# Kernel tuning notes

Measured on AMD Instinct MI355X. Metric: run time of the kernel, lower is better.

Reference implementation:

```python
import jax, jax.numpy as jnp
import numpy as np
import math

D = 768      # n_embd
NH = 12      # n_head
L = 4        # n_layer
E = 8        # num_experts
K = 2        # top_k
V = 50257    # vocab
H = 4 * D    # ffn hidden
MOE_LAYERS = (1, 3)


def _ln(x, g, b):
    m = x.mean(-1, keepdims=True)
    v = ((x - m) ** 2).mean(-1, keepdims=True)
    return (x - m) * jax.lax.rsqrt(v + 1e-5) * g + b


def setup_inputs() -> dict:
    key = jax.random.key(0)
    ks = iter(jax.random.split(key, 32))
    s = 0.02

    def rnd(shape):
        return jax.random.normal(next(ks), shape, dtype=jnp.float32) * s

    inp = {
        "x": jax.random.randint(next(ks), (2, 512), 0, V),
        "emb": rnd((V, D)),                       # tied embedding / output projection
        "wqkv": rnd((L, 3 * D, D)), "bqkv": jnp.zeros((L, 3 * D)),
        "wo": rnd((L, D, D)), "bo": jnp.zeros((L, D)),
        "ln1g": jnp.ones((L, D)), "ln1b": jnp.zeros((L, D)),
        "ln2g": jnp.ones((L, D)), "ln2b": jnp.zeros((L, D)),
        "sw1": rnd((2, H, D)), "sb1": jnp.zeros((2, H)),   # dense FFN layers (0, 2)
        "sw2": rnd((2, D, H)), "sb2": jnp.zeros((2, D)),
        "gw": rnd((2, E, D)),                              # router weights (layers 1, 3)
        "mw1": rnd((2, E, H, D)), "mb1": jnp.zeros((2, E, H)),
        "mw2": rnd((2, E, D, H)), "mb2": jnp.zeros((2, E, D)),
        "lnfg": jnp.ones((D,)), "lnfb": jnp.zeros((D,)),
    }
    return inp


def reference(x, emb, wqkv, bqkv, wo, bo, ln1g, ln1b, ln2g, ln2b,
              sw1, sb1, sw2, sb2, gw, mw1, mb1, mw2, mb2, lnfg, lnfb):
    b, t = x.shape
    dh = D // NH

    h = emb[x]  # [b,t,d]
    # sinusoidal positional encoding
    pos = jnp.arange(t, dtype=jnp.float32)[:, None]
    div = jnp.exp(jnp.arange(0, D, 2, dtype=jnp.float32) * (-math.log(10000.0) / D))
    pe = jnp.stack([jnp.sin(pos * div), jnp.cos(pos * div)], axis=-1).reshape(t, D)
    h = h + pe[None]

    # causal mask: query i cannot attend to key j > i
    neg = jnp.asarray(-jnp.inf, dtype=h.dtype)
    mask = jnp.where(jnp.arange(t)[None, :] > jnp.arange(t)[:, None], neg, 0.0)

    std_i = 0
    moe_i = 0
    for i in range(L):
        # pre-norm self-attention
        xn = _ln(h, ln1g[i], ln1b[i])
        qkv = xn @ wqkv[i].T + bqkv[i]          # [b,t,3d]
        q, k, v = jnp.split(qkv, 3, axis=-1)

        def heads(z):
            return z.reshape(b, t, NH, dh).transpose(0, 2, 1, 3)  # [b,nh,t,dh]

        q, k, v = heads(q), heads(k), heads(v)
        sc = jnp.einsum('bhqd,bhkd->bhqk', q, k) / math.sqrt(dh) + mask
        a = jax.nn.softmax(sc, axis=-1)
        o = jnp.einsum('bhqk,bhkd->bhqd', a, v).transpose(0, 2, 1, 3).reshape(b, t, D)
        h = h + o @ wo[i].T + bo[i]

        # pre-norm FFN (dense or MoE)
        xn = _ln(h, ln2g[i], ln2b[i])
        if i in MOE_LAYERS:
            T = b * t
            xf = xn.reshape(T, D)
            gl = xf @ gw[moe_i].T                      # router logits [T,E]
            probs = jax.nn.softmax(gl, axis=-1)
            topv, topi = jax.lax.top_k(probs, K)       # [T,K]
            w = topv / topv.sum(-1, keepdims=True)     # renormalized top-k gates
            cw = jnp.zeros_like(probs).at[jnp.arange(T)[:, None], topi].set(w)  # [T,E]
            he = jax.nn.gelu(jnp.einsum('td,ehd->teh', xf, mw1[moe_i]) + mb1[moe_i],
                             approximate=False)        # [T,E,H]
            ye = jnp.einsum('teh,edh->ted', he, mw2[moe_i]) + mb2[moe_i]        # [T,E,D]
            ff = jnp.einsum('ted,te->td', ye, cw).reshape(b, t, D)
            moe_i += 1
        else:
            ff = jax.nn.gelu(xn @ sw1[std_i].T + sb1[std_i], approximate=False) @ sw2[std_i].T + sb2[std_i]
            std_i += 1
        h = h + ff

    h = _ln(h, lnfg, lnfb)
    logits = h @ emb.T  # tied output projection, [b,t,V]
    return logits
```

## Files before the change

### kernel.cpp

```cpp
#include <hip/hip_runtime.h>
#include <hip/hip_bf16.h>
#include <cstdint>
#include <cstddef>

#define Dm   768
#define NHm  12
#define Lm   4
#define Em   8
#define Vm   50257
#define Hm   3072
#define Tm   512
#define Bm   2
#define NT   (Bm*Tm)
#define NAS  (NT*2)

typedef float f32x4 __attribute__((ext_vector_type(4)));
typedef short bf16x8 __attribute__((ext_vector_type(8)));

__device__ __forceinline__ float gelu_exact(float x) {
    return 0.5f * x * (1.0f + erff(x * 0.70710678118654752440f));
}

__device__ __forceinline__ unsigned short f2bf(float f) {
    __hip_bfloat16 h = __float2bfloat16(f);
    union { __hip_bfloat16 h; unsigned short s; } c; c.h = h; return c.s;
}
__device__ __forceinline__ float bf2f_bits(unsigned short b) {
    union { unsigned u; float f; } c; c.u = ((unsigned)b) << 16; return c.f;
}

__global__ __launch_bounds__(256) void cvt_bf16_kernel(const float* __restrict__ in,
                                                       unsigned short* __restrict__ out,
                                                       long n) {
    long i = ((long)blockIdx.x * 256 + threadIdx.x) * 8;
    if (i + 8 <= n) {
        const float4* s4 = reinterpret_cast<const float4*>(in + i);
        float4 f0 = s4[0], f1 = s4[1];
        union { unsigned short s[8]; uint4 v; } p;
        p.s[0] = f2bf(f0.x); p.s[1] = f2bf(f0.y); p.s[2] = f2bf(f0.z); p.s[3] = f2bf(f0.w);
        p.s[4] = f2bf(f1.x); p.s[5] = f2bf(f1.y); p.s[6] = f2bf(f1.z); p.s[7] = f2bf(f1.w);
        *reinterpret_cast<uint4*>(out + i) = p.v;
    } else {
        for (long j = i; j < n; ++j) out[j] = f2bf(in[j]);
    }
}

__global__ __launch_bounds__(256) void embed_kernel(const int* __restrict__ x,
                                                    const float* __restrict__ emb,
                                                    float* __restrict__ h) {
    int g = blockIdx.x;
    int tid = threadIdx.x;
    int tok = x[g];
    int pos = g % Tm;
    const float* erow = emb + (size_t)tok * Dm;
    for (int d = tid; d < Dm; d += 256) {
        int i2 = (d >> 1) * 2;
        float div = expf(-logf(10000.0f) * (float)i2 / (float)Dm);
        float a = (float)pos * div;
        float pe = (d & 1) ? cosf(a) : sinf(a);
        h[(size_t)g * Dm + d] = erow[d] + pe;
    }
}

__global__ __launch_bounds__(256) void ln_kernel(const float* __restrict__ in,
                                                 const float* __restrict__ g,
                                                 const float* __restrict__ b,
                                                 float* __restrict__ out) {
    int t = blockIdx.x, tid = threadIdx.x;
    const float* x = in + (size_t)t * Dm;
    float v0 = x[tid], v1 = x[tid + 256], v2 = x[tid + 512];
    __shared__ float red[256];
    red[tid] = v0 + v1 + v2;
    __syncthreads();
    for (int off = 128; off > 0; off >>= 1) {
        if (tid < off) red[tid] += red[tid + off];
        __syncthreads();
    }
    float mean = red[0] * (1.0f / Dm);
    __syncthreads();
    float d0 = v0 - mean, d1 = v1 - mean, d2 = v2 - mean;
    red[tid] = d0 * d0 + d1 * d1 + d2 * d2;
    __syncthreads();
    for (int off = 128; off > 0; off >>= 1) {
        if (tid < off) red[tid] += red[tid + off];
        __syncthreads();
    }
    float inv = rsqrtf(red[0] * (1.0f / Dm) + 1e-5f);
    float* o = out + (size_t)t * Dm;
    o[tid]       = d0 * inv * g[tid]       + b[tid];
    o[tid + 256] = d1 * inv * g[tid + 256] + b[tid + 256];
    o[tid + 512] = d2 * inv * g[tid + 512] + b[tid + 512];
}

#define MB 128
#define NB 128
#define KB 32
#define LDT 40

__device__ __forceinline__ void stage_tile(unsigned short* lds, const float* src,
                                           bool valid, int srow, int shalf) {
    union { unsigned short s[8]; uint4 v; } p0, p1;
    if (valid) {
        const float4* s4 = reinterpret_cast<const float4*>(src);
        #pragma unroll
        for (int q = 0; q < 4; ++q) {
            float4 f = s4[q];
            float vv[4] = {f.x, f.y, f.z, f.w};
            #pragma unroll
            for (int j = 0; j < 4; ++j) {
                int idx = q * 4 + j;
                unsigned short hb = f2bf(vv[j]);
                if (idx < 8) p0.s[idx] = hb; else p1.s[idx - 8] = hb;
            }
        }
    } else {
        p0.v = make_uint4(0, 0, 0, 0);
        p1.v = make_uint4(0, 0, 0, 0);
    }
    uint4* dst = reinterpret_cast<uint4*>(&lds[srow * LDT + shalf * 16]);
    dst[0] = p0.v; dst[1] = p1.v;
}

__device__ __forceinline__ void stage_tile_split(unsigned short* lds_hi,
                                                 unsigned short* lds_lo,
                                                 const float* src,
                                                 bool valid, int srow, int shalf) {
    union { unsigned short s[8]; uint4 v; } h0, h1, l0, l1;
    if (valid) {
        const float4* s4 = reinterpret_cast<const float4*>(src);
        #pragma unroll
        for (int q = 0; q < 4; ++q) {
            float4 f = s4[q];
            float vv[4] = {f.x, f.y, f.z, f.w};
            #pragma unroll
            for (int j = 0; j < 4; ++j) {
                int idx = q * 4 + j;
                unsigned short hb = f2bf(vv[j]);
                unsigned short lb = f2bf(vv[j] - bf2f_bits(hb));
                if (idx < 8) { h0.s[idx] = hb; l0.s[idx] = lb; }
                else         { h1.s[idx - 8] = hb; l1.s[idx - 8] = lb; }
            }
        }
    } else {
        h0.v = make_uint4(0,0,0,0); h1.v = make_uint4(0,0,0,0);
        l0.v = make_uint4(0,0,0,0); l1.v = make_uint4(0,0,0,0);
    }
    uint4* dh = reinterpret_cast<uint4*>(&lds_hi[srow * LDT + shalf * 16]);
    dh[0] = h0.v; dh[1] = h1.v;
    uint4* dl = reinterpret_cast<uint4*>(&lds_lo[srow * LDT + shalf * 16]);
    dl[0] = l0.v; dl[1] = l1.v;
}

__global__ __launch_bounds__(256) void mfma_gemm_bf(const unsigned short* __restrict__ A,
                                                    const unsigned short* __restrict__ B,
                                                    const float* __restrict__ bias,
                                                    float* __restrict__ C,
                                                    int M, int N, int K) {
    __shared__ __align__(16) unsigned short As[MB * LDT];
    __shared__ __align__(16) unsigned short Bs[NB * LDT];
    int tid = threadIdx.x;
    int nt_m = M / MB;
    int total = gridDim.x;
    int bid = blockIdx.x;
    int swz = bid;
    if ((total & 7) == 0) {
        int chunk = total >> 3;
        swz = (bid & 7) * chunk + (bid >> 3);
    }
    int bm = (swz % nt_m) * MB;
    int bn = (swz / nt_m) * NB;
    int srow = tid >> 1, shalf = tid & 1;
    int lane = tid & 63, w = tid >> 6;
    int wr = w >> 1, wc = w & 1;
    int r0 = (lane >> 4) * 4, c0 = lane & 15;
    int kb = (lane >> 4) * 8;

    bool bval = (bn + srow) < N;
    const unsigned short* Ap = A + (size_t)(bm + srow) * K + shalf * 16;
    const unsigned short* Bp = B + (size_t)(bn + srow) * K + shalf * 16;

    uint4 ra0, ra1, rb0, rb1;
    ra0 = reinterpret_cast<const uint4*>(Ap)[0];
    ra1 = reinterpret_cast<const uint4*>(Ap)[1];
    rb0 = make_uint4(0,0,0,0); rb1 = make_uint4(0,0,0,0);
    if (bval) {
        rb0 = reinterpret_cast<const uint4*>(Bp)[0];
        rb1 = reinterpret_cast<const uint4*>(Bp)[1];
    }

    f32x4 acc[4][4] = {};

    for (int kk = 0; kk < K; kk += KB) {
        uint4* da = reinterpret_cast<uint4*>(&As[srow * LDT + shalf * 16]);
        da[0] = ra0; da[1] = ra1;
        uint4* db = reinterpret_cast<uint4*>(&Bs[srow * LDT + shalf * 16]);
        db[0] = rb0; db[1] = rb1;
        __syncthreads();
        if (kk + KB < K) {
            const uint4* na = reinterpret_cast<const uint4*>(Ap + kk + KB);
            ra0 = na[0]; ra1 = na[1];
            if (bval) {
                const uint4* nb = reinterpret_cast<const uint4*>(Bp + kk + KB);
                rb0 = nb[0]; rb1 = nb[1];
            }
        }
        bf16x8 af[4], bf[4];
        #pragma unroll
        for (int m = 0; m < 4; ++m)
            af[m] = *reinterpret_cast<const bf16x8*>(&As[(wr * 64 + m * 16 + c0) * LDT + kb]);
        #pragma unroll
        for (int n = 0; n < 4; ++n)
            bf[n] = *reinterpret_cast<const bf16x8*>(&Bs[(wc * 64 + n * 16 + c0) * LDT + kb]);
        #pragma unroll
        for (int m = 0; m < 4; ++m)
            #pragma unroll
            for (int n = 0; n < 4; ++n)
                acc[m][n] = __builtin_amdgcn_mfma_f32_16x16x32_bf16(af[m], bf[n], acc[m][n], 0, 0, 0);
        __syncthreads();
    }

    #pragma unroll
    for (int n = 0; n < 4; ++n) {
        int col = bn + wc * 64 + n * 16 + c0;
        if (col < N) {
            float bv = bias ? bias[col] : 0.f;
            #pragma unroll
            for (int m = 0; m < 4; ++m)
                #pragma unroll
                for (int r = 0; r < 4; ++r) {
                    int row = bm + wr * 64 + m * 16 + r0 + r;
                    C[(size_t)row * N + col] = acc[m][n][r] + bv;
                }
        }
    }
}

template<int ACT, int RES>
__global__ __launch_bounds__(256) void mfma_gemm(const float* __restrict__ A,
                                                 const float* __restrict__ B,
                                                 const float* __restrict__ bias,
                                                 const float* __restrict__ res,
                                                 float* __restrict__ C,
                                                 int M, int N, int K) {
    __shared__ __align__(16) unsigned short As[MB * LDT];
    __shared__ __align__(16) unsigned short Bs[NB * LDT];
    int tid = threadIdx.x;
    int bm = blockIdx.y * MB, bn = blockIdx.x * NB;
    int srow = tid >> 1, shalf = tid & 1;
    int lane = tid & 63, w = tid >> 6;
    int wr = w >> 1, wc = w & 1;
    int r0 = (lane >> 4) * 4, c0 = lane & 15;
    int kb = (lane >> 4) * 8;

    f32x4 acc[4][4] = {};

    for (int kk = 0; kk < K; kk += KB) {
        stage_tile(As, A + (size_t)(bm + srow) * K + kk + shalf * 16, true, srow, shalf);
        bool bval = (bn + srow) < N;
        stage_tile(Bs, B + (size_t)(bn + srow) * K + kk + shalf * 16, bval, srow, shalf);
        __syncthreads();
        bf16x8 af[4], bf[4];
        #pragma unroll
        for (int m = 0; m < 4; ++m)
            af[m] = *reinterpret_cast<const bf16x8*>(&As[(wr * 64 + m * 16 + c0) * LDT + kb]);
        #pragma unroll
        for (int n = 0; n < 4; ++n)
            bf[n] = *reinterpret_cast<const bf16x8*>(&Bs[(wc * 64 + n * 16 + c0) * LDT + kb]);
        #pragma unroll
        for (int m = 0; m < 4; ++m)
            #pragma unroll
            for (int n = 0; n < 4; ++n)
                acc[m][n] = __builtin_amdgcn_mfma_f32_16x16x32_bf16(af[m], bf[n], acc[m][n], 0, 0, 0);
        __syncthreads();
    }

    #pragma unroll
    for (int n = 0; n < 4; ++n) {
        int col = bn + wc * 64 + n * 16 + c0;
        if (col < N) {
            float bv = bias ? bias[col] : 0.f;
            #pragma unroll
            for (int m = 0; m < 4; ++m) {
                #pragma unroll
                for (int r = 0; r < 4; ++r) {
                    int row = bm + wr * 64 + m * 16 + r0 + r;
                    float v = acc[m][n][r] + bv;
                    if (RES) v += res[(size_t)row * N + col];
                    if (ACT == 1) v = gelu_exact(v);
                    C[(size_t)row * N + col] = v;
                }
            }
        }
    }
}

__global__ __launch_bounds__(256) void mfma_gemm_sp_part(const float* __restrict__ A,
                                                         const float* __restrict__ B,
                                                         float* __restrict__ part,
                                                         int M, int N, int K, int KSPLIT) {
    __shared__ __align__(16) unsigned short Ah[MB * LDT];
    __shared__ __align__(16) unsigned short Al[MB * LDT];
    __shared__ __align__(16) unsigned short Bh[NB * LDT];
    __shared__ __align__(16) unsigned short Bl[NB * LDT];
    int tid = threadIdx.x;
    int bm = blockIdx.y * MB, bn = blockIdx.x * NB;
    int kc = blockIdx.z;
    int chunk = K / KSPLIT;
    int kbeg = kc * chunk;
    int srow = tid >> 1, shalf = tid & 1;
    int lane = tid & 63, w = tid >> 6;
    int wr = w >> 1, wc = w & 1;
    int r0 = (lane >> 4) * 4, c0 = lane & 15;
    int kb = (lane >> 4) * 8;

    f32x4 acc[4][4] = {};

    for (int kk = kbeg; kk < kbeg + chunk; kk += KB) {
        stage_tile_split(Ah, Al, A + (size_t)(bm + srow) * K + kk + shalf * 16, true, srow, shalf);
        stage_tile_split(Bh, Bl, B + (size_t)(bn + srow) * K + kk + shalf * 16, true, srow, shalf);
        __syncthreads();
        bf16x8 ah[4], al[4], bh[4], bl[4];
        #pragma unroll
        for (int m = 0; m < 4; ++m) {
            int o = (wr * 64 + m * 16 + c0) * LDT + kb;
            ah[m] = *reinterpret_cast<const bf16x8*>(&Ah[o]);
            al[m] = *reinterpret_cast<const bf16x8*>(&Al[o]);
        }
        #pragma unroll
        for (int n = 0; n < 4; ++n) {
            int o = (wc * 64 + n * 16 + c0) * LDT + kb;
            bh[n] = *reinterpret_cast<const bf16x8*>(&Bh[o]);
            bl[n] = *reinterpret_cast<const bf16x8*>(&Bl[o]);
        }
        #pragma unroll
        for (int m = 0; m < 4; ++m)
            #pragma unroll
            for (int n = 0; n < 4; ++n) {
                acc[m][n] = __builtin_amdgcn_mfma_f32_16x16x32_bf16(al[m], bh[n], acc[m][n], 0, 0, 0);
                acc[m][n] = __builtin_amdgcn_mfma_f32_16x16x32_bf16(ah[m], bl[n], acc[m][n], 0, 0, 0);
                acc[m][n] = __builtin_amdgcn_mfma_f32_16x16x32_bf16(ah[m], bh[n], acc[m][n], 0, 0, 0);
            }
        __syncthreads();
    }

    float* P = part + (size_t)kc * M * N;
    #pragma unroll
    for (int n = 0; n < 4; ++n) {
        int col = bn + wc * 64 + n * 16 + c0;
        #pragma unroll
        for (int m = 0; m < 4; ++m)
            #pragma unroll
            for (int r = 0; r < 4; ++r) {
                int row = bm + wr * 64 + m * 16 + r0 + r;
                P[(size_t)row * N + col] = acc[m][n][r];
            }
    }
}

template<int ACT, int RES>
__global__ __launch_bounds__(256) void reduce_dense(const float* __restrict__ part,
                                                    const float* __restrict__ bias,
                                                    const float* __restrict__ res,
                                                    float* __restrict__ C,
                                                    long MN, int N, int KSPLIT) {
    long stride = (long)gridDim.x * 256 * 4;
    for (long i = ((long)blockIdx.x * 256 + threadIdx.x) * 4; i < MN; i += stride) {
        float4 v = *reinterpret_cast<const float4*>(part + i);
        for (int kc = 1; kc < KSPLIT; ++kc) {
            float4 p = *reinterpret_cast<const float4*>(part + (size_t)kc * MN + i);
            v.x += p.x; v.y += p.y; v.z += p.z; v.w += p.w;
        }
        int col = (int)(i % N);
        float4 b = *reinterpret_cast<const float4*>(bias + col);
        v.x += b.x; v.y += b.y; v.z += b.z; v.w += b.w;
        if (RES) {
            float4 r = *reinterpret_cast<const float4*>(res + i);
            v.x += r.x; v.y += r.y; v.z += r.z; v.w += r.w;
        }
        if (ACT == 1) {
            v.x = gelu_exact(v.x); v.y = gelu_exact(v.y);
            v.z = gelu_exact(v.z); v.w = gelu_exact(v.w);
        }
        *reinterpret_cast<float4*>(C + i) = v;
    }
}

#define LDA 72
__device__ __forceinline__ void stage16a(unsigned short* dh, unsigned short* dl,
                                         const float* src) {
    union { unsigned short s[8]; uint4 v; } h0, h1, l0, l1;
    const float4* s4 = reinterpret_cast<const float4*>(src);
    #pragma unroll
    for (int q = 0; q < 4; ++q) {
        float4 f = s4[q];
        float vv[4] = {f.x, f.y, f.z, f.w};
        #pragma unroll
        for (int j = 0; j < 4; ++j) {
            int idx = q * 4 + j;
            unsigned short hb = f2bf(vv[j]);
            unsigned short lb = f2bf(vv[j] - bf2f_bits(hb));
            if (idx < 8) { h0.s[idx] = hb; l0.s[idx] = lb; }
            else         { h1.s[idx - 8] = hb; l1.s[idx - 8] = lb; }
        }
    }
    reinterpret_cast<uint4*>(dh)[0] = h0.v; reinterpret_cast<uint4*>(dh)[1] = h1.v;
    reinterpret_cast<uint4*>(dl)[0] = l0.v; reinterpret_cast<uint4*>(dl)[1] = l1.v;
}

__global__ __launch_bounds__(256) void attn_flash(const float* __restrict__ qkv,
                                                  float* __restrict__ o_out) {
    int qt = blockIdx.x;
    int bh = blockIdx.y;
    int b = bh / NHm, hh = bh % NHm;
    const int g0 = b * Tm;
    const int hoff = hh * 64;
    int tid = threadIdx.x;
    int lane = tid & 63, w = tid >> 6;
    int c0 = lane & 15, hi4 = lane >> 4;
    int kb = hi4 * 8;

    __shared__ __align__(16) unsigned short Qh[64 * LDA], Ql[64 * LDA];
    __shared__ __align__(16) unsigned short Kh[64 * LDA], Kl[64 * LDA];
    __shared__ __align__(16) unsigned short Vh[64 * LDA], Vl[64 * LDA];
    __shared__ __align__(16) unsigned short Ph[4][16 * LDA], Pl[4][16 * LDA];

    {
        int srow = tid >> 2, q = tid & 3;
        stage16a(&Qh[srow * LDA + q * 16], &Ql[srow * LDA + q * 16],
                 qkv + (size_t)(g0 + qt * 64 + srow) * (3 * Dm) + hoff + q * 16);
    }
    __syncthreads();

    f32x4 acc_o[4] = {};
    float m_r[4] = {-1e30f, -1e30f, -1e30f, -1e30f};
    float l_r[4] = {0.f, 0.f, 0.f, 0.f};

    for (int kt = 0; kt <= qt; ++kt) {
        {
            int srow = tid >> 2, q = tid & 3;
            stage16a(&Kh[srow * LDA + q * 16], &Kl[srow * LDA + q * 16],
                     qkv + (size_t)(g0 + kt * 64 + srow) * (3 * Dm) + Dm + hoff + q * 16);
        }
        {
            int d = lane, kg = w;
            const float* vbase = qkv + (size_t)(g0 + kt * 64 + kg * 16) * (3 * Dm) + 2 * Dm + hoff + d;
            #pragma unroll
            for (int k2 = 0; k2 < 16; ++k2) {
                float v = vbase[(size_t)k2 * (3 * Dm)];
                unsigned short hb = f2bf(v);
                Vh[d * LDA + kg * 16 + k2] = hb;
                Vl[d * LDA + kg * 16 + k2] = f2bf(v - bf2f_bits(hb));
            }
        }
        __syncthreads();

        f32x4 sAcc[4] = {};
        #pragma unroll
        for (int kk2 = 0; kk2 < 64; kk2 += 32) {
            bf16x8 ah = *reinterpret_cast<const bf16x8*>(&Qh[(w * 16 + c0) * LDA + kk2 + kb]);
            bf16x8 al = *reinterpret_cast<const bf16x8*>(&Ql[(w * 16 + c0) * LDA + kk2 + kb]);
            #pragma unroll
            for (int n = 0; n < 4; ++n) {
                bf16x8 bh_ = *reinterpret_cast<const bf16x8*>(&Kh[(n * 16 + c0) * LDA + kk2 + kb]);
                bf16x8 bl_ = *reinterpret_cast<const bf16x8*>(&Kl[(n * 16 + c0) * LDA + kk2 + kb]);
                sAcc[n] = __builtin_amdgcn_mfma_f32_16x16x32_bf16(al, bh_, sAcc[n], 0, 0, 0);
                sAcc[n] = __builtin_amdgcn_mfma_f32_16x16x32_bf16(ah, bl_, sAcc[n], 0, 0, 0);
                sAcc[n] = __builtin_amdgcn_mfma_f32_16x16x32_bf16(ah, bh_, sAcc[n], 0, 0, 0);
            }
        }

        float p[4][4];
        float smax[4] = {-3e38f, -3e38f, -3e38f, -3e38f};
        #pragma unroll
        for (int n = 0; n < 4; ++n)
            #pragma unroll
            for (int r = 0; r < 4; ++r) {
                float s = sAcc[n][r] * 0.125f;
                if (kt == qt) {
                    int kg = n * 16 + c0;
                    int qg = w * 16 + hi4 * 4 + r;
                    if (kg > qg) s = -3e38f;
                }
                p[n][r] = s;
                smax[r] = fmaxf(smax[r], s);
            }
        #pragma unroll
        for (int off = 1; off < 16; off <<= 1)
            #pragma unroll
            for (int r = 0; r < 4; ++r)
                smax[r] = fmaxf(smax[r], __shfl_xor(smax[r], off));
        float f_r[4], lsum[4];
        #pragma unroll
        for (int r = 0; r < 4; ++r) {
            float mn = fmaxf(m_r[r], smax[r]);
            f_r[r] = expf(m_r[r] - mn);
            m_r[r] = mn;
        }
        #pragma unroll
        for (int n = 0; n < 4; ++n)
            #pragma unroll
            for (int r = 0; r < 4; ++r)
                p[n][r] = expf(p[n][r] - m_r[r]);
        #pragma unroll
        for (int r = 0; r < 4; ++r)
            lsum[r] = p[0][r] + p[1][r] + p[2][r] + p[3][r];
        #pragma unroll
        for (int off = 1; off < 16; off <<= 1)
            #pragma unroll
            for (int r = 0; r < 4; ++r)
                lsum[r] += __shfl_xor(lsum[r], off);
        #pragma unroll
        for (int r = 0; r < 4; ++r)
            l_r[r] = l_r[r] * f_r[r] + lsum[r];
        #pragma unroll
        for (int n = 0; n < 4; ++n)
            #pragma unroll
            for (int r = 0; r < 4; ++r)
                acc_o[n][r] *= f_r[r];

        #pragma unroll
        for (int n = 0; n < 4; ++n)
            #pragma unroll
            for (int r = 0; r < 4; ++r) {
                unsigned short hb = f2bf(p[n][r]);
                int o = (hi4 * 4 + r) * LDA + n * 16 + c0;
                Ph[w][o] = hb;
                Pl[w][o] = f2bf(p[n][r] - bf2f_bits(hb));
            }

        #pragma unroll
        for (int kk2 = 0; kk2 < 64; kk2 += 32) {
            bf16x8 pah = *reinterpret_cast<const bf16x8*>(&Ph[w][c0 * LDA + kk2 + kb]);
            bf16x8 pal = *reinterpret_cast<const bf16x8*>(&Pl[w][c0 * LDA + kk2 + kb]);
            #pragma unroll
            for (int n = 0; n < 4; ++n) {
                bf16x8 vbh = *reinterpret_cast<const bf16x8*>(&Vh[(n * 16 + c0) * LDA + kk2 + kb]);
                bf16x8 vbl = *reinterpret_cast<const bf16x8*>(&Vl[(n * 16 + c0) * LDA + kk2 + kb]);
                acc_o[n] = __builtin_amdgcn_mfma_f32_16x16x32_bf16(pal, vbh, acc_o[n], 0, 0, 0);
                acc_o[n] = __builtin_amdgcn_mfma_f32_16x16x32_bf16(pah, vbl, acc_o[n], 0, 0, 0);
                acc_o[n] = __builtin_amdgcn_mfma_f32_16x16x32_bf16(pah, vbh, acc_o[n], 0, 0, 0);
            }
        }
        __syncthreads();
    }

    float inv[4];
    #pragma unroll
    for (int r = 0; r < 4; ++r) inv[r] = 1.0f / l_r[r];
    #pragma unroll
    for (int n = 0; n < 4; ++n)
        #pragma unroll
        for (int r = 0; r < 4; ++r) {
            int row = g0 + qt * 64 + w * 16 + hi4 * 4 + r;
            o_out[(size_t)row * Dm + hoff + n * 16 + c0] = acc_o[n][r] * inv[r];
        }
}

__global__ __launch_bounds__(256) void router_kernel(const float* __restrict__ xn,
                                                     const float* __restrict__ gw,
                                                     int* __restrict__ topi,
                                                     float* __restrict__ topw) {
    int t = blockIdx.x * 4 + (threadIdx.x >> 6);
    int lane = threadIdx.x & 63;
    const float4* x4 = reinterpret_cast<const float4*>(xn + (size_t)t * Dm);
    float4 xv[3];
    #pragma unroll
    for (int i = 0; i < 3; ++i) xv[i] = x4[lane + i * 64];

    float l[Em];
    #pragma unroll
    for (int e = 0; e < Em; ++e) {
        const float4* w4 = reinterpret_cast<const float4*>(gw + (size_t)e * Dm);
        float dot = 0.f;
        #pragma unroll
        for (int i = 0; i < 3; ++i) {
            float4 wv = w4[lane + i * 64];
            dot += xv[i].x * wv.x + xv[i].y * wv.y + xv[i].z * wv.z + xv[i].w * wv.w;
        }
        #pragma unroll
        for (int off = 32; off > 0; off >>= 1) dot += __shfl_xor(dot, off);
        l[e] = dot;
    }
    if (lane == 0) {
        int i1 = 0;
        #pragma unroll
        for (int e = 1; e < Em; ++e) if (l[e] > l[i1]) i1 = e;
        int i2 = (i1 == 0) ? 1 : 0;
        #pragma unroll
        for (int e = 0; e < Em; ++e) if (e != i1 && l[e] > l[i2]) i2 = e;
        float w1 = 1.0f / (1.0f + expf(l[i2] - l[i1]));
        topi[t * 2] = i1; topi[t * 2 + 1] = i2;
        topw[t * 2] = w1; topw[t * 2 + 1] = 1.0f - w1;
    }
}

__global__ __launch_bounds__(256) void route_build_kernel(const int* __restrict__ topi,
                                                          int* __restrict__ g_cnt,
                                                          int* __restrict__ g_off,
                                                          int* __restrict__ bucket) {
    __shared__ int cnt[Em], off[Em], pos[Em];
    int tid = threadIdx.x;
    if (tid < Em) cnt[tid] = 0;
    __syncthreads();
    for (int ts = tid; ts < NAS; ts += 256) atomicAdd(&cnt[topi[ts]], 1);
    __syncthreads();
    if (tid == 0) {
        int acc = 0;
        for (int e = 0; e < Em; ++e) { off[e] = acc; pos[e] = acc; acc += cnt[e]; }
    }
    __syncthreads();
    for (int ts = tid; ts < NAS; ts += 256) {
        int e = topi[ts];
        int p = atomicAdd(&pos[e], 1);
        bucket[p] = ts;
    }
    if (tid < Em) { g_cnt[tid] = cnt[tid]; g_off[tid] = off[tid]; }
}

template<int SPLIT>
__global__ __launch_bounds__(256) void moe_mfma_gemm1(const float* __restrict__ xn,
                                                      const float* __restrict__ W1all,
                                                      const float* __restrict__ B1all,
                                                      const int* __restrict__ bucket,
                                                      const int* __restrict__ cnt,
                                                      const int* __restrict__ off,
                                                      float* __restrict__ heg) {
    int e = blockIdx.z;
    int count = cnt[e];
    int mbase = blockIdx.y * MB;
    if (mbase >= count) return;
    int base = off[e];

    __shared__ __align__(16) unsigned short Ah[MB * LDT];
    __shared__ __align__(16) unsigned short Bh[NB * LDT];
    __shared__ __align__(16) unsigned short Al[SPLIT ? MB * LDT : 8];
    __shared__ __align__(16) unsigned short Bl[SPLIT ? NB * LDT : 8];
    __shared__ int toks[MB];
    int tid = threadIdx.x;
    int bn = blockIdx.x * NB;
    int srow = tid >> 1, shalf = tid & 1;
    int lane = tid & 63, w = tid >> 6;
    int wr = w >> 1, wc = w & 1;
    int r0 = (lane >> 4) * 4, c0 = lane & 15;
    int kb = (lane >> 4) * 8;
    if (tid < MB) {
        int p = mbase + tid;
        toks[tid] = (p < count) ? (bucket[base + p] >> 1) : -1;
    }
    __syncthreads();

    f32x4 acc[4][4] = {};
    const float* W = W1all + (size_t)e * Hm * Dm;
    int t = toks[srow];
    for (int kk = 0; kk < Dm; kk += KB) {
        if (SPLIT) {
            stage_tile_split(Ah, Al, xn + (size_t)t * Dm + kk + shalf * 16, t >= 0, srow, shalf);
            stage_tile_split(Bh, Bl, W + (size_t)(bn + srow) * Dm + kk + shalf * 16, true, srow, shalf);
        } else {
            stage_tile(Ah, xn + (size_t)t * Dm + kk + shalf * 16, t >= 0, srow, shalf);
            stage_tile(Bh, W + (size_t)(bn + srow) * Dm + kk + shalf * 16, true, srow, shalf);
        }
        __syncthreads();
        bf16x8 ah[4], bh[4], al[4], bl[4];
        #pragma unroll
        for (int m = 0; m < 4; ++m) {
            int o = (wr * 64 + m * 16 + c0) * LDT + kb;
            ah[m] = *reinterpret_cast<const bf16x8*>(&Ah[o]);
            if (SPLIT) al[m] = *reinterpret_cast<const bf16x8*>(&Al[o]);
        }
        #pragma unroll
        for (int n = 0; n < 4; ++n) {
            int o = (wc * 64 + n * 16 + c0) * LDT + kb;
            bh[n] = *reinterpret_cast<const bf16x8*>(&Bh[o]);
            if (SPLIT) bl[n] = *reinterpret_cast<const bf16x8*>(&Bl[o]);
        }
        #pragma unroll
        for (int m = 0; m < 4; ++m)
            #pragma unroll
            for (int n = 0; n < 4; ++n) {
                if (SPLIT) {
                    acc[m][n] = __builtin_amdgcn_mfma_f32_16x16x32_bf16(al[m], bh[n], acc[m][n], 0, 0, 0);
                    acc[m][n] = __builtin_amdgcn_mfma_f32_16x16x32_bf16(ah[m], bl[n], acc[m][n], 0, 0, 0);
                }
                acc[m][n] = __builtin_amdgcn_mfma_f32_16x16x32_bf16(ah[m], bh[n], acc[m][n], 0, 0, 0);
            }
        __syncthreads();
    }

    const float* b1 = B1all + (size_t)e * Hm;
    #pragma unroll
    for (int n = 0; n < 4; ++n) {
        int col = bn + wc * 64 + n * 16 + c0;
        float bv = b1[col];
        #pragma unroll
        for (int m = 0; m < 4; ++m) {
            #pragma unroll
            for (int r = 0; r < 4; ++r) {
                int p = mbase + wr * 64 + m * 16 + r0 + r;
                if (p < count)
                    heg[(size_t)(base + p) * Hm + col] = gelu_exact(acc[m][n][r] + bv);
            }
        }
    }
}

template<int SPLIT>
__global__ __launch_bounds__(256) void moe_gemm2_part(const float* __restrict__ heg,
                                                      const float* __restrict__ W2all,
                                                      const int* __restrict__ cnt,
                                                      const int* __restrict__ off,
                                                      float* __restrict__ part,
                                                      int KSPLIT) {
    int e = blockIdx.z;
    int count = cnt[e];
    int my = blockIdx.y;
    int kc = my % KSPLIT, mb = my / KSPLIT;
    int mbase = mb * MB;
    if (mbase >= count) return;
    int base = off[e];
    int chunk = Hm / KSPLIT;
    int kbeg = kc * chunk;

    __shared__ __align__(16) unsigned short Ah[MB * LDT];
    __shared__ __align__(16) unsigned short Bh[NB * LDT];
    __shared__ __align__(16) unsigned short Al[SPLIT ? MB * LDT : 8];
    __shared__ __align__(16) unsigned short Bl[SPLIT ? NB * LDT : 8];
    int tid = threadIdx.x;
    int bn = blockIdx.x * NB;
    int srow = tid >> 1, shalf = tid & 1;
    int lane = tid & 63, w = tid >> 6;
    int wr = w >> 1, wc = w & 1;
    int r0 = (lane >> 4) * 4, c0 = lane & 15;
    int kb = (lane >> 4) * 8;

    f32x4 acc[4][4] = {};
    const float* W = W2all + (size_t)e * Dm * Hm;
    bool aval = (mbase + srow) < count;
    for (int kk = kbeg; kk < kbeg + chunk; kk += KB) {
        if (SPLIT) {
            stage_tile_split(Ah, Al, heg + (size_t)(base + mbase + srow) * Hm + kk + shalf * 16, aval, srow, shalf);
            stage_tile_split(Bh, Bl, W + (size_t)(bn + srow) * Hm + kk + shalf * 16, true, srow, shalf);
        } else {
            stage_tile(Ah, heg + (size_t)(base + mbase + srow) * Hm + kk + shalf * 16, aval, srow, shalf);
            stage_tile(Bh, W + (size_t)(bn + srow) * Hm + kk + shalf * 16, true, srow, shalf);
        }
        __syncthreads();
        bf16x8 ah[4], bh[4], al[4], bl[4];
        #pragma unroll
        for (int m = 0; m < 4; ++m) {
            int o = (wr * 64 + m * 16 + c0) * LDT + kb;
            ah[m] = *reinterpret_cast<const bf16x8*>(&Ah[o]);
            if (SPLIT) al[m] = *reinterpret_cast<const bf16x8*>(&Al[o]);
        }
        #pragma unroll
        for (int n = 0; n < 4; ++n) {
            int o = (wc * 64 + n * 16 + c0) * LDT + kb;
            bh[n] = *reinterpret_cast<const bf16x8*>(&Bh[o]);
            if (SPLIT) bl[n] = *reinterpret_cast<const bf16x8*>(&Bl[o]);
        }
        #pragma unroll
        for (int m = 0; m < 4; ++m)
            #pragma unroll
            for (int n = 0; n < 4; ++n) {
                if (SPLIT) {
                    acc[m][n] = __builtin_amdgcn_mfma_f32_16x16x32_bf16(al[m], bh[n], acc[m][n], 0, 0, 0);
                    acc[m][n] = __builtin_amdgcn_mfma_f32_16x16x32_bf16(ah[m], bl[n], acc[m][n], 0, 0, 0);
                }
                acc[m][n] = __builtin_amdgcn_mfma_f32_16x16x32_bf16(ah[m], bh[n], acc[m][n], 0, 0, 0);
            }
        __syncthreads();
    }

    float* P = part + (size_t)kc * NAS * Dm;
    #pragma unroll
    for (int n = 0; n < 4; ++n) {
        int col = bn + wc * 64 + n * 16 + c0;
        #pragma unroll
        for (int m = 0; m < 4; ++m) {
            #pragma unroll
            for (int r = 0; r < 4; ++r) {
                int p = mbase + wr * 64 + m * 16 + r0 + r;
                if (p < count)
                    P[(size_t)(base + p) * Dm + col] = acc[m][n][r];
            }
        }
    }
}

__global__ __launch_bounds__(256) void moe_reduce(const float* __restrict__ part,
                                                  const float* __restrict__ B2all,
                                                  const int* __restrict__ bucket,
                                                  const int* __restrict__ topi,
                                                  const float* __restrict__ topw,
                                                  float* __restrict__ ye, int KSPLIT) {
    const long MN = (long)NAS * Dm;
    long stride = (long)gridDim.x * 256 * 4;
    for (long i = ((long)blockIdx.x * 256 + threadIdx.x) * 4; i < MN; i += stride) {
        int p = (int)(i / Dm), col = (int)(i % Dm);
        int ts = bucket[p];
        int e = topi[ts];
        float wgt = topw[ts];
        float4 v = *reinterpret_cast<const float4*>(part + i);
        for (int kc = 1; kc < KSPLIT; ++kc) {
            float4 q = *reinterpret_cast<const float4*>(part + (size_t)kc * MN + i);
            v.x += q.x; v.y += q.y; v.z += q.z; v.w += q.w;
        }
        float4 b = *reinterpret_cast<const float4*>(B2all + (size_t)e * Dm + col);
        float4 o;
        o.x = wgt * (v.x + b.x); o.y = wgt * (v.y + b.y);
        o.z = wgt * (v.z + b.z); o.w = wgt * (v.w + b.w);
        *reinterpret_cast<float4*>(ye + (size_t)ts * Dm + col) = o;
    }
}

__global__ __launch_bounds__(256) void combine_kernel(float* __restrict__ h,
                                                      const float* __restrict__ ye) {
    int i = blockIdx.x * 256 + threadIdx.x;
    if (i < NT * Dm) {
        int t = i / Dm, d = i - t * Dm;
        h[i] += ye[(size_t)(t * 2) * Dm + d] + ye[(size_t)(t * 2 + 1) * Dm + d];
    }
}

extern "C" void kernel_launch(void* const* d_in, const int* in_sizes, int n_in,
                              void* d_out, int out_size, void* d_ws, size_t ws_size,
                              hipStream_t stream) {
    const int*   x    = (const int*)d_in[0];
    const float* emb  = (const float*)d_in[1];
    const float* wqkv = (const float*)d_in[2];
    const float* bqkv = (const float*)d_in[3];
    const float* wo   = (const float*)d_in[4];
    const float* bo   = (const float*)d_in[5];
    const float* ln1g = (const float*)d_in[6];
    const float* ln1b = (const float*)d_in[7];
    const float* ln2g = (const float*)d_in[8];
    const float* ln2b = (const float*)d_in[9];
    const float* sw1  = (const float*)d_in[10];
    const float* sb1  = (const float*)d_in[11];
    const float* sw2  = (const float*)d_in[12];
    const float* sb2  = (const float*)d_in[13];
    const float* gw   = (const float*)d_in[14];
    const float* mw1  = (const float*)d_in[15];
    const float* mb1  = (const float*)d_in[16];
    const float* mw2  = (const float*)d_in[17];
    const float* mb2  = (const float*)d_in[18];
    const float* lnfg = (const float*)d_in[19];
    const float* lnfb = (const float*)d_in[20];

    const size_t n_h    = (size_t)NT * Dm;
    const size_t n_qkv  = (size_t)NT * 3 * Dm;
    const size_t n_ffh  = (size_t)NT * Hm;
    const size_t n_ye   = (size_t)NAS * Dm;
    const size_t n_heg  = (size_t)NAS * Hm;
    const size_t n_xn   = (size_t)NT * Dm;
    const size_t n_part = (size_t)NT * Hm * 2;
    const size_t n_embbf = (size_t)Vm * Dm / 2;
    const size_t n_xnbf  = (size_t)NT * Dm / 2;
    const size_t n_big   = n_h + n_qkv + n_h + n_ffh + n_ye + n_heg + n_part;

    size_t wsf = ws_size / sizeof(float);

    float* w = (float*)d_ws;
    float* xn   = w;            w += n_xn;
    float* topw = w;            w += NAS;
    int*   topi = (int*)w;      w += NAS;
    int*   bucket = (int*)w;    w += NAS;
    int*   e_cnt = (int*)w;     w += 8;
    int*   e_off = (int*)w;     w += 8;
    size_t used = (size_t)(w - (float*)d_ws);

    unsigned short* emb_bf = nullptr;
    unsigned short* xn_bf  = nullptr;
    if (wsf >= used + n_embbf + n_xnbf + 64) {
        emb_bf = (unsigned short*)w;  w += n_embbf;
        xn_bf  = (unsigned short*)w;  w += n_xnbf;
        used = (size_t)(w - (float*)d_ws);
    }

    float *h, *qkv, *attno, *ffh, *ye, *heg, *part;
    if (wsf >= used + n_big + 64) {
        float* a = w;
        h = a;      a += n_h;
        qkv = a;    a += n_qkv;
        attno = a;  a += n_h;
        ffh = a;    a += n_ffh;
        ye = a;     a += n_ye;
        heg = a;    a += n_heg;
        part = a;
    } else {
        float* a = (float*)d_out;
        h = a;      a += n_h;
        qkv = a;    a += n_qkv;
        attno = a;  a += n_h;
        ffh = a;    a += n_ffh;
        ye = a;     a += n_ye;
        heg = a;    a += n_heg;
        part = a;
    }

    if (emb_bf) {
        long n = (long)Vm * Dm;
        cvt_bf16_kernel<<<(unsigned)((n / 8 + 255) / 256), 256, 0, stream>>>(emb, emb_bf, n);
    }

    embed_kernel<<<NT, 256, 0, stream>>>(x, emb, h);

    const int RBLK = 2048;
    int std_i = 0, moe_i = 0;
    for (int l = 0; l < Lm; ++l) {
        ln_kernel<<<NT, 256, 0, stream>>>(h, ln1g + l * Dm, ln1b + l * Dm, xn);
        mfma_gemm_sp_part<<<dim3((3 * Dm) / NB, NT / MB, 2), 256, 0, stream>>>(
            xn, wqkv + (size_t)l * 3 * Dm * Dm, part, NT, 3 * Dm, Dm, 2);
        reduce_dense<0,0><<<RBLK, 256, 0, stream>>>(
            part, bqkv + (size_t)l * 3 * Dm, nullptr, qkv, (long)NT * 3 * Dm, 3 * Dm, 2);
        attn_flash<<<dim3(Tm / 64, Bm * NHm), 256, 0, stream>>>(qkv, attno);
        mfma_gemm_sp_part<<<dim3(Dm / NB, NT / MB, 4), 256, 0, stream>>>(
            attno, wo + (size_t)l * Dm * Dm, part, NT, Dm, Dm, 4);
        reduce_dense<0,1><<<RBLK, 256, 0, stream>>>(
            part, bo + (size_t)l * Dm, h, h, (long)NT * Dm, Dm, 4);

        ln_kernel<<<NT, 256, 0, stream>>>(h, ln2g + l * Dm, ln2b + l * Dm, xn);
        if (l == 1 || l == 3) {
            router_kernel<<<NT / 4, 256, 0, stream>>>(
                xn, gw + (size_t)moe_i * Em * Dm, topi, topw);
            route_build_kernel<<<1, 256, 0, stream>>>(topi, e_cnt, e_off, bucket);
            if (l == 3) {
                moe_mfma_gemm1<0><<<dim3(Hm / NB, NAS / MB, Em), 256, 0, stream>>>(
                    xn, mw1 + (size_t)moe_i * Em * Hm * Dm, mb1 + (size_t)moe_i * Em * Hm,
                    bucket, e_cnt, e_off, heg);
                moe_gemm2_part<0><<<dim3(Dm / NB, (NAS / MB) * 4, Em), 256, 0, stream>>>(
                    heg, mw2 + (size_t)moe_i * Em * Dm * Hm, e_cnt, e_off, part, 4);
            } else {
                moe_mfma_gemm1<1><<<dim3(Hm / NB, NAS / MB, Em), 256, 0, stream>>>(
                    xn, mw1 + (size_t)moe_i * Em * Hm * Dm, mb1 + (size_t)moe_i * Em * Hm,
                    bucket, e_cnt, e_off, heg);
                moe_gemm2_part<1><<<dim3(Dm / NB, (NAS / MB) * 4, Em), 256, 0, stream>>>(
                    heg, mw2 + (size_t)moe_i * Em * Dm * Hm, e_cnt, e_off, part, 4);
            }
            moe_reduce<<<RBLK, 256, 0, stream>>>(
                part, mb2 + (size_t)moe_i * Em * Dm, bucket, topi, topw, ye, 4);
            combine_kernel<<<(NT * Dm) / 256, 256, 0, stream>>>(h, ye);
            moe_i++;
        } else {
            mfma_gemm_sp_part<<<dim3(Hm / NB, NT / MB, 2), 256, 0, stream>>>(
                xn, sw1 + (size_t)std_i * Hm * Dm, part, NT, Hm, Dm, 2);
            reduce_dense<1,0><<<RBLK, 256, 0, stream>>>(
                part, sb1 + (size_t)std_i * Hm, nullptr, ffh, (long)NT * Hm, Hm, 2);
            mfma_gemm_sp_part<<<dim3(Dm / NB, NT / MB, 8), 256, 0, stream>>>(
                ffh, sw2 + (size_t)std_i * Dm * Hm, part, NT, Dm, Hm, 8);
            reduce_dense<0,1><<<RBLK, 256, 0, stream>>>(
                part, sb2 + (size_t)std_i * Dm, h, h, (long)NT * Dm, Dm, 8);
            std_i++;
        }
    }

    ln_kernel<<<NT, 256, 0, stream>>>(h, lnfg, lnfb, xn);
    if (emb_bf) {
        long n = (long)NT * Dm;
        cvt_bf16_kernel<<<(unsigned)((n / 8 + 255) / 256), 256, 0, stream>>>(xn, xn_bf, n);
        int nblk = (NT / MB) * ((Vm + NB - 1) / NB);
        mfma_gemm_bf<<<dim3(nblk), 256, 0, stream>>>(
            xn_bf, emb_bf, nullptr, (float*)d_out, NT, Vm, Dm);
    } else {
        mfma_gemm<0,0><<<dim3((Vm + NB - 1) / NB, NT / MB), 256, 0, stream>>>(
            xn, emb, nullptr, nullptr, (float*)d_out, NT, Vm, Dm);
    }
}
```

Measured before the change: 1.126 ms.

## Fuse residual reductions with layernorm and stage GEMM epilogues through LDS

Split-K reductions that add bias and residual now also compute the following layernorm in the same kernel, and the MoE combine is likewise fused with the next layernorm. This removes the separate ln_kernel launches and their extra pass over the hidden state. The split-K partial GEMM and the bf16 logits GEMM now transpose accumulators through shared memory so each lane writes contiguous float4 stores instead of scattered scalar stores. The per-row fused kernels run one block per token with tree reductions, and the LDS-staged epilogue adds extra shared-memory traffic.

```diff
diff --git a/kernel.cpp b/kernel.cpp
--- a/kernel.cpp
+++ b/kernel.cpp
@@ -156,8 +156,9 @@
                                                     const float* __restrict__ bias,
                                                     float* __restrict__ C,
                                                     int M, int N, int K) {
-    __shared__ __align__(16) unsigned short As[MB * LDT];
-    __shared__ __align__(16) unsigned short Bs[NB * LDT];
+    __shared__ __align__(16) unsigned short SMEM[2 * MB * LDT];
+    unsigned short* As = SMEM;
+    unsigned short* Bs = SMEM + MB * LDT;
     int tid = threadIdx.x;
     int nt_m = M / MB;
     int total = gridDim.x;
@@ -219,18 +220,32 @@
         __syncthreads();
     }
 
-    #pragma unroll
-    for (int n = 0; n < 4; ++n) {
-        int col = bn + wc * 64 + n * 16 + c0;
-        if (col < N) {
-            float bv = bias ? bias[col] : 0.f;
-            #pragma unroll
-            for (int m = 0; m < 4; ++m)
+    float* Ct = reinterpret_cast<float*>(SMEM);
+    float* cw = Ct + w * 1024;
+    #pragma unroll
+    for (int m = 0; m < 4; ++m) {
+        #pragma unroll
+        for (int n = 0; n < 4; ++n)
+            #pragma unroll
+            for (int r = 0; r < 4; ++r)
+                cw[(r0 + r) * 64 + n * 16 + c0] = acc[m][n][r];
+        #pragma unroll
+        for (int ch = 0; ch < 4; ++ch) {
+            f32x4 vv = *reinterpret_cast<const f32x4*>(&cw[ch * 256 + lane * 4]);
+            int rg = bm + wr * 64 + m * 16 + ch * 4 + (lane >> 4);
+            int cg = bn + wc * 64 + (lane & 15) * 4;
+            if (cg + 3 < N) {
+                if (bias) {
+                    vv[0] += bias[cg]; vv[1] += bias[cg + 1];
+                    vv[2] += bias[cg + 2]; vv[3] += bias[cg + 3];
+                }
+                *reinterpret_cast<f32x4*>(&C[(size_t)rg * N + cg]) = vv;
+            } else {
                 #pragma unroll
-                for (int r = 0; r < 4; ++r) {
-                    int row = bm + wr * 64 + m * 16 + r0 + r;
-                    C[(size_t)row * N + col] = acc[m][n][r] + bv;
-                }
+                for (int e = 0; e < 4; ++e)
+                    if (cg + e < N)
+                        C[(size_t)rg * N + cg + e] = vv[e] + (bias ? bias[cg + e] : 0.f);
+            }
         }
     }
 }
@@ -298,10 +313,11 @@
                                                          const float* __restrict__ B,
                                                          float* __restrict__ part,
                                                          int M, int N, int K, int KSPLIT) {
-    __shared__ __align__(16) unsigned short Ah[MB * LDT];
-    __shared__ __align__(16) unsigned short Al[MB * LDT];
-    __shared__ __align__(16) unsigned short Bh[NB * LDT];
-    __shared__ __align__(16) unsigned short Bl[NB * LDT];
+    __shared__ __align__(16) unsigned short SMEM[4 * MB * LDT];
+    unsigned short* Ah = SMEM;
+    unsigned short* Al = SMEM + MB * LDT;
+    unsigned short* Bh = SMEM + 2 * MB * LDT;
+    unsigned short* Bl = SMEM + 3 * MB * LDT;
     int tid = threadIdx.x;
     int bm = blockIdx.y * MB, bn = blockIdx.x * NB;
     int kc = blockIdx.z;
@@ -343,24 +359,29 @@
         __syncthreads();
     }
 
+    float* Ct = reinterpret_cast<float*>(SMEM);
+    float* cw = Ct + w * 1024;
     float* P = part + (size_t)kc * M * N;
     #pragma unroll
-    for (int n = 0; n < 4; ++n) {
-        int col = bn + wc * 64 + n * 16 + c0;
-        #pragma unroll
-        for (int m = 0; m < 4; ++m)
-            #pragma unroll
-            for (int r = 0; r < 4; ++r) {
-                int row = bm + wr * 64 + m * 16 + r0 + r;
-                P[(size_t)row * N + col] = acc[m][n][r];
-            }
-    }
-}
-
-template<int ACT, int RES>
+    for (int m = 0; m < 4; ++m) {
+        #pragma unroll
+        for (int n = 0; n < 4; ++n)
+            #pragma unroll
+            for (int r = 0; r < 4; ++r)
+                cw[(r0 + r) * 64 + n * 16 + c0] = acc[m][n][r];
+        #pragma unroll
+        for (int ch = 0; ch < 4; ++ch) {
+            f32x4 vv = *reinterpret_cast<const f32x4*>(&cw[ch * 256 + lane * 4]);
+            int rg = bm + wr * 64 + m * 16 + ch * 4 + (lane >> 4);
+            int cg = bn + wc * 64 + (lane & 15) * 4;
+            *reinterpret_cast<f32x4*>(&P[(size_t)rg * N + cg]) = vv;
+        }
+    }
+}
+
+template<int ACT>
 __global__ __launch_bounds__(256) void reduce_dense(const float* __restrict__ part,
                                                     const float* __restrict__ bias,
-                                                    const float* __restrict__ res,
                                                     float* __restrict__ C,
                                                     long MN, int N, int KSPLIT) {
     long stride = (long)gridDim.x * 256 * 4;
@@ -373,16 +394,93 @@
         int col = (int)(i % N);
         float4 b = *reinterpret_cast<const float4*>(bias + col);
         v.x += b.x; v.y += b.y; v.z += b.z; v.w += b.w;
-        if (RES) {
-            float4 r = *reinterpret_cast<const float4*>(res + i);
-            v.x += r.x; v.y += r.y; v.z += r.z; v.w += r.w;
-        }
         if (ACT == 1) {
             v.x = gelu_exact(v.x); v.y = gelu_exact(v.y);
             v.z = gelu_exact(v.z); v.w = gelu_exact(v.w);
         }
         *reinterpret_cast<float4*>(C + i) = v;
     }
+}
+
+__global__ __launch_bounds__(256) void reduce_ln(const float* __restrict__ part,
+                                                 const float* __restrict__ bias,
+                                                 float* __restrict__ h,
+                                                 const float* __restrict__ g,
+                                                 const float* __restrict__ b,
+                                                 float* __restrict__ xn,
+                                                 int KSPLIT) {
+    const long MN = (long)NT * Dm;
+    int t = blockIdx.x, tid = threadIdx.x;
+    float v[3];
+    #pragma unroll
+    for (int j = 0; j < 3; ++j) {
+        int col = tid + j * 256;
+        long idx = (long)t * Dm + col;
+        float s = part[idx];
+        for (int kc = 1; kc < KSPLIT; ++kc) s += part[(size_t)kc * MN + idx];
+        s += bias[col] + h[idx];
+        h[idx] = s;
+        v[j] = s;
+    }
+    __shared__ float red[256];
+    red[tid] = v[0] + v[1] + v[2];
+    __syncthreads();
+    for (int off = 128; off > 0; off >>= 1) {
+        if (tid < off) red[tid] += red[tid + off];
+        __syncthreads();
+    }
+    float mean = red[0] * (1.0f / Dm);
+    __syncthreads();
+    float d0 = v[0] - mean, d1 = v[1] - mean, d2 = v[2] - mean;
+    red[tid] = d0 * d0 + d1 * d1 + d2 * d2;
+    __syncthreads();
+    for (int off = 128; off > 0; off >>= 1) {
+        if (tid < off) red[tid] += red[tid + off];
+        __syncthreads();
+    }
+    float inv = rsqrtf(red[0] * (1.0f / Dm) + 1e-5f);
+    float* o = xn + (size_t)t * Dm;
+    o[tid]       = d0 * inv * g[tid]       + b[tid];
+    o[tid + 256] = d1 * inv * g[tid + 256] + b[tid + 256];
+    o[tid + 512] = d2 * inv * g[tid + 512] + b[tid + 512];
+}
+
+__global__ __launch_bounds__(256) void combine_ln(float* __restrict__ h,
+                                                  const float* __restrict__ ye,
+                                                  const float* __restrict__ g,
+                                                  const float* __restrict__ b,
+                                                  float* __restrict__ xn) {
+    int t = blockIdx.x, tid = threadIdx.x;
+    float v[3];
+    #pragma unroll
+    for (int j = 0; j < 3; ++j) {
+        int col = tid + j * 256;
+        long idx = (long)t * Dm + col;
+        float s = h[idx] + ye[(size_t)(t * 2) * Dm + col] + ye[(size_t)(t * 2 + 1) * Dm + col];
+        h[idx] = s;
+        v[j] = s;
+    }
+    __shared__ float red[256];
+    red[tid] = v[0] + v[1] + v[2];
+    __syncthreads();
+    for (int off = 128; off > 0; off >>= 1) {
+        if (tid < off) red[tid] += red[tid + off];
+        __syncthreads();
+    }
+    float mean = red[0] * (1.0f / Dm);
+    __syncthreads();
+    float d0 = v[0] - mean, d1 = v[1] - mean, d2 = v[2] - mean;
+    red[tid] = d0 * d0 + d1 * d1 + d2 * d2;
+    __syncthreads();
+    for (int off = 128; off > 0; off >>= 1) {
+        if (tid < off) red[tid] += red[tid + off];
+        __syncthreads();
+    }
+    float inv = rsqrtf(red[0] * (1.0f / Dm) + 1e-5f);
+    float* o = xn + (size_t)t * Dm;
+    o[tid]       = d0 * inv * g[tid]       + b[tid];
+    o[tid + 256] = d1 * inv * g[tid + 256] + b[tid + 256];
+    o[tid + 512] = d2 * inv * g[tid + 512] + b[tid + 512];
 }
 
 #define LDA 72
@@ -810,15 +908,6 @@
         o.x = wgt * (v.x + b.x); o.y = wgt * (v.y + b.y);
         o.z = wgt * (v.z + b.z); o.w = wgt * (v.w + b.w);
         *reinterpret_cast<float4*>(ye + (size_t)ts * Dm + col) = o;
-    }
-}
-
-__global__ __launch_bounds__(256) void combine_kernel(float* __restrict__ h,
-                                                      const float* __restrict__ ye) {
-    int i = blockIdx.x * 256 + threadIdx.x;
-    if (i < NT * Dm) {
-        int t = i / Dm, d = i - t * Dm;
-        h[i] += ye[(size_t)(t * 2) * Dm + d] + ye[(size_t)(t * 2 + 1) * Dm + d];
     }
 }
 
@@ -904,22 +993,24 @@
     }
 
     embed_kernel<<<NT, 256, 0, stream>>>(x, emb, h);
+    ln_kernel<<<NT, 256, 0, stream>>>(h, ln1g, ln1b, xn);
 
     const int RBLK = 2048;
     int std_i = 0, moe_i = 0;
     for (int l = 0; l < Lm; ++l) {
-        ln_kernel<<<NT, 256, 0, stream>>>(h, ln1g + l * Dm, ln1b + l * Dm, xn);
+        const float* ng = (l < 3) ? (ln1g + (l + 1) * Dm) : lnfg;
+        const float* nb = (l < 3) ? (ln1b + (l + 1) * Dm) : lnfb;
+
         mfma_gemm_sp_part<<<dim3((3 * Dm) / NB, NT / MB, 2), 256, 0, stream>>>(
             xn, wqkv + (size_t)l * 3 * Dm * Dm, part, NT, 3 * Dm, Dm, 2);
-        reduce_dense<0,0><<<RBLK, 256, 0, stream>>>(
-            part, bqkv + (size_t)l * 3 * Dm, nullptr, qkv, (long)NT * 3 * Dm, 3 * Dm, 2);
+        reduce_dense<0><<<RBLK, 256, 0, stream>>>(
+            part, bqkv + (size_t)l * 3 * Dm, qkv, (long)NT * 3 * Dm, 3 * Dm, 2);
         attn_flash<<<dim3(Tm / 64, Bm * NHm), 256, 0, stream>>>(qkv, attno);
         mfma_gemm_sp_part<<<dim3(Dm / NB, NT / MB, 4), 256, 0, stream>>>(
             attno, wo + (size_t)l * Dm * Dm, part, NT, Dm, Dm, 4);
-        reduce_dense<0,1><<<RBLK, 256, 0, stream>>>(
-            part, bo + (size_t)l * Dm, h, h, (long)NT * Dm, Dm, 4);
-
-        ln_kernel<<<NT, 256, 0, stream>>>(h, ln2g + l * Dm, ln2b + l * Dm, xn);
+        reduce_ln<<<NT, 256, 0, stream>>>(
+            part, bo + (size_t)l * Dm, h, ln2g + l * Dm, ln2b + l * Dm, xn, 4);
+
         if (l == 1 || l == 3) {
             router_kernel<<<NT / 4, 256, 0, stream>>>(
                 xn, gw + (size_t)moe_i * Em * Dm, topi, topw);
@@ -939,22 +1030,21 @@
             }
             moe_reduce<<<RBLK, 256, 0, stream>>>(
                 part, mb2 + (size_t)moe_i * Em * Dm, bucket, topi, topw, ye, 4);
-            combine_kernel<<<(NT * Dm) / 256, 256, 0, stream>>>(h, ye);
+            combine_ln<<<NT, 256, 0, stream>>>(h, ye, ng, nb, xn);
             moe_i++;
         } else {
             mfma_gemm_sp_part<<<dim3(Hm / NB, NT / MB, 2), 256, 0, stream>>>(
                 xn, sw1 + (size_t)std_i * Hm * Dm, part, NT, Hm, Dm, 2);
-            reduce_dense<1,0><<<RBLK, 256, 0, stream>>>(
-                part, sb1 + (size_t)std_i * Hm, nullptr, ffh, (long)NT * Hm, Hm, 2);
+            reduce_dense<1><<<RBLK, 256, 0, stream>>>(
+                part, sb1 + (size_t)std_i * Hm, ffh, (long)NT * Hm, Hm, 2);
             mfma_gemm_sp_part<<<dim3(Dm / NB, NT / MB, 8), 256, 0, stream>>>(
                 ffh, sw2 + (size_t)std_i * Dm * Hm, part, NT, Dm, Hm, 8);
-            reduce_dense<0,1><<<RBLK, 256, 0, stream>>>(
-                part, sb2 + (size_t)std_i * Dm, h, h, (long)NT * Dm, Dm, 8);
+            reduce_ln<<<NT, 256, 0, stream>>>(
+                part, sb2 + (size_t)std_i * Dm, h, ng, nb, xn, 8);
             std_i++;
         }
     }
 
-    ln_kernel<<<NT, 256, 0, stream>>>(h, lnfg, lnfb, xn);
     if (emb_bf) {
         long n = (long)NT * Dm;
         cvt_bf16_kernel<<<(unsigned)((n / 8 + 255) / 256), 256, 0, stream>>>(xn, xn_bf, n);
```

Result: faster. 1.068 ms (-5.2%).
